# Optimization experiments

Measured on AMD Instinct MI355X. Metric: run time of the kernel, lower is better.

## Reference

```python
import jax, jax.numpy as jnp
import numpy as np

EPS = 1e-05

def setup_inputs() -> dict:
    key = jax.random.key(0)
    k1, = jax.random.split(key, 1)
    x = jax.random.normal(k1, (4, 4096, 2048), dtype=jnp.float32)
    g = jnp.ones((2048,), dtype=jnp.float32)
    return {"x": x, "g": g}

def reference(x, g):
    # RMSNorm: x / sqrt(mean(x^2, axis=-1) + eps) * g, computed in fp32
    dtype = x.dtype
    xf = x.astype(jnp.float32)
    ms = jnp.mean(xf * xf, axis=-1, keepdims=True)  # [B,S,1]
    out = xf * jax.lax.rsqrt(ms + EPS) * g
    return out.astype(dtype)
```

## Files before the change

kernel.cpp:

```cpp
#include <hip/hip_runtime.h>

#define ROW_LEN 2048
#define BLOCK   256
#define EPS     1e-5f

__global__ __launch_bounds__(BLOCK) void RMSNorm_56607668961691_kernel(
    const float* __restrict__ x,
    const float* __restrict__ g,
    float* __restrict__ out)
{
    const int row = blockIdx.x;
    const int tid = threadIdx.x;

    const float4* __restrict__ xr   = reinterpret_cast<const float4*>(x + (size_t)row * ROW_LEN);
    float4* __restrict__       outr = reinterpret_cast<float4*>(out + (size_t)row * ROW_LEN);
    const float4* __restrict__ gv   = reinterpret_cast<const float4*>(g);

    float4 a = xr[tid];
    float4 b = xr[tid + BLOCK];

    float ss = a.x * a.x + a.y * a.y + a.z * a.z + a.w * a.w
             + b.x * b.x + b.y * b.y + b.z * b.z + b.w * b.w;

    #pragma unroll
    for (int off = 32; off > 0; off >>= 1)
        ss += __shfl_down(ss, off, 64);

    __shared__ float wave_sums[BLOCK / 64];
    const int wave = tid >> 6;
    const int lane = tid & 63;
    if (lane == 0) wave_sums[wave] = ss;
    __syncthreads();

    const float total = wave_sums[0] + wave_sums[1] + wave_sums[2] + wave_sums[3];
    const float scale = rsqrtf(total * (1.0f / (float)ROW_LEN) + EPS);

    const float4 ga = gv[tid];
    const float4 gb = gv[tid + BLOCK];

    float4 oa, ob;
    oa.x = a.x * scale * ga.x;
    oa.y = a.y * scale * ga.y;
    oa.z = a.z * scale * ga.z;
    oa.w = a.w * scale * ga.w;
    ob.x = b.x * scale * gb.x;
    ob.y = b.y * scale * gb.y;
    ob.z = b.z * scale * gb.z;
    ob.w = b.w * scale * gb.w;

    outr[tid]         = oa;
    outr[tid + BLOCK] = ob;
}

extern "C" void kernel_launch(void* const* d_in, const int* in_sizes, int n_in,
                              void* d_out, int out_size, void* d_ws, size_t ws_size,
                              hipStream_t stream) {
    const float* x = (const float*)d_in[0];
    const float* g = (const float*)d_in[1];
    float* out = (float*)d_out;

    const int rows = in_sizes[0] / ROW_LEN;
    RMSNorm_56607668961691_kernel<<<rows, BLOCK, 0, stream>>>(x, g, out);
}
```

Measured before the change: 227.6 us.

## Map one wave per row and drop block-level reduction sync

Each 64-lane wave now processes a whole row, with every lane loading eight float4 values and reducing via xor shuffles, so the shared-memory exchange and __syncthreads are removed. Four rows are packed per block. Outputs are written with nontemporal stores to reduce cache pollution. This raises per-lane register use and memory-level parallelism per wave, in exchange for fewer threads per row.

```diff
diff --git a/kernel.cpp b/kernel.cpp
--- a/kernel.cpp
+++ b/kernel.cpp
@@ -1,64 +1,63 @@
 #include <hip/hip_runtime.h>
 
 #define ROW_LEN 2048
-#define BLOCK   256
-#define EPS     1e-5f
+#define WAVES_PER_BLOCK 4
+#define BLOCK (WAVES_PER_BLOCK * 64)
+#define V4_PER_LANE (ROW_LEN / 4 / 64)
+#define EPS 1e-5f
+
+typedef float vf4 __attribute__((ext_vector_type(4)));
 
 __global__ __launch_bounds__(BLOCK) void RMSNorm_56607668961691_kernel(
-    const float* __restrict__ x,
-    const float* __restrict__ g,
-    float* __restrict__ out)
+    const vf4* __restrict__ x,
+    const vf4* __restrict__ g,
+    vf4* __restrict__ out,
+    int rows)
 {
-    const int row = blockIdx.x;
-    const int tid = threadIdx.x;
+    const int wave = threadIdx.x >> 6;
+    const int lane = threadIdx.x & 63;
+    const int row  = blockIdx.x * WAVES_PER_BLOCK + wave;
+    if (row >= rows) return;
 
-    const float4* __restrict__ xr   = reinterpret_cast<const float4*>(x + (size_t)row * ROW_LEN);
-    float4* __restrict__       outr = reinterpret_cast<float4*>(out + (size_t)row * ROW_LEN);
-    const float4* __restrict__ gv   = reinterpret_cast<const float4*>(g);
+    const vf4* __restrict__ xr   = x   + (size_t)row * (ROW_LEN / 4);
+    vf4* __restrict__       outr = out + (size_t)row * (ROW_LEN / 4);
 
-    float4 a = xr[tid];
-    float4 b = xr[tid + BLOCK];
+    vf4 v[V4_PER_LANE];
+    #pragma unroll
+    for (int k = 0; k < V4_PER_LANE; ++k)
+        v[k] = xr[lane + k * 64];
 
-    float ss = a.x * a.x + a.y * a.y + a.z * a.z + a.w * a.w
-             + b.x * b.x + b.y * b.y + b.z * b.z + b.w * b.w;
+    float ss = 0.0f;
+    #pragma unroll
+    for (int k = 0; k < V4_PER_LANE; ++k)
+        ss += v[k].x * v[k].x + v[k].y * v[k].y + v[k].z * v[k].z + v[k].w * v[k].w;
 
     #pragma unroll
     for (int off = 32; off > 0; off >>= 1)
-        ss += __shfl_down(ss, off, 64);
+        ss += __shfl_xor(ss, off, 64);
 
-    __shared__ float wave_sums[BLOCK / 64];
-    const int wave = tid >> 6;
-    const int lane = tid & 63;
-    if (lane == 0) wave_sums[wave] = ss;
-    __syncthreads();
+    const float scale = rsqrtf(ss * (1.0f / (float)ROW_LEN) + EPS);
 
-    const float total = wave_sums[0] + wave_sums[1] + wave_sums[2] + wave_sums[3];
-    const float scale = rsqrtf(total * (1.0f / (float)ROW_LEN) + EPS);
-
-    const float4 ga = gv[tid];
-    const float4 gb = gv[tid + BLOCK];
-
-    float4 oa, ob;
-    oa.x = a.x * scale * ga.x;
-    oa.y = a.y * scale * ga.y;
-    oa.z = a.z * scale * ga.z;
-    oa.w = a.w * scale * ga.w;
-    ob.x = b.x * scale * gb.x;
-    ob.y = b.y * scale * gb.y;
-    ob.z = b.z * scale * gb.z;
-    ob.w = b.w * scale * gb.w;
-
-    outr[tid]         = oa;
-    outr[tid + BLOCK] = ob;
+    #pragma unroll
+    for (int k = 0; k < V4_PER_LANE; ++k) {
+        vf4 gk = g[lane + k * 64];
+        vf4 o;
+        o.x = v[k].x * scale * gk.x;
+        o.y = v[k].y * scale * gk.y;
+        o.z = v[k].z * scale * gk.z;
+        o.w = v[k].w * scale * gk.w;
+        __builtin_nontemporal_store(o, &outr[lane + k * 64]);
+    }
 }
 
 extern "C" void kernel_launch(void* const* d_in, const int* in_sizes, int n_in,
                               void* d_out, int out_size, void* d_ws, size_t ws_size,
                               hipStream_t stream) {
-    const float* x = (const float*)d_in[0];
-    const float* g = (const float*)d_in[1];
-    float* out = (float*)d_out;
+    const vf4* x = (const vf4*)d_in[0];
+    const vf4* g = (const vf4*)d_in[1];
+    vf4* out = (vf4*)d_out;
 
     const int rows = in_sizes[0] / ROW_LEN;
-    RMSNorm_56607668961691_kernel<<<rows, BLOCK, 0, stream>>>(x, g, out);
+    const int grid = (rows + WAVES_PER_BLOCK - 1) / WAVES_PER_BLOCK;
+    RMSNorm_56607668961691_kernel<<<grid, BLOCK, 0, stream>>>(x, g, out, rows);
 }
```

Measured after the change: 231.9 us. No clear change (+1.9%).
